# Kernel tuning notes

Measured on AMD Instinct MI355X. Metric: run time of the kernel, lower is better.

## Reference

```python
import jax, jax.numpy as jnp
import numpy as np

FEATURE_DIM = 512
PREDICATE_DIM = 2000
OBJECT_DIM = 100000
BATCH = 131072
EPS = 1e-5


def setup_inputs() -> dict:
    key = jax.random.key(0)
    ks = jax.random.split(key, 20)
    f, f2 = FEATURE_DIM, FEATURE_DIM // 2

    def w(k, shape, fan_in):
        bound = 1.0 / np.sqrt(fan_in)
        return jax.random.uniform(k, shape, jnp.float32, -bound, bound)

    inp = {
        "subj": jax.random.randint(ks[0], (BATCH,), 0, OBJECT_DIM),
        "obj": jax.random.randint(ks[1], (BATCH,), 0, OBJECT_DIM),
        "predi": jax.random.randint(ks[2], (BATCH,), 0, PREDICATE_DIM),
        # Linear weights stored as (in, out) so one_hot @ W.T == W_io[idx]
        "W1": w(ks[3], (OBJECT_DIM, f), OBJECT_DIM), "b1": w(ks[4], (f,), OBJECT_DIM),
        "g1": jnp.ones((f,), jnp.float32), "be1": jnp.zeros((f,), jnp.float32),
        "W2": w(ks[5], (OBJECT_DIM, f), OBJECT_DIM), "b2": w(ks[6], (f,), OBJECT_DIM),
        "g2": jnp.ones((f,), jnp.float32), "be2": jnp.zeros((f,), jnp.float32),
        "W3": w(ks[7], (PREDICATE_DIM, f), PREDICATE_DIM), "b3": w(ks[8], (f,), PREDICATE_DIM),
        "g3": jnp.ones((f,), jnp.float32), "be3": jnp.zeros((f,), jnp.float32),
        "W4": w(ks[9], (f2, f), f), "b4": w(ks[10], (f2,), f),
        "g4": jnp.ones((f2,), jnp.float32), "be4": jnp.zeros((f2,), jnp.float32),
        "W5": w(ks[11], (1, f2), f2), "b5": w(ks[12], (1,), f2),
    }
    return inp


def _bn(x, g, b):
    # BatchNorm1d training mode: biased variance over batch
    m = jnp.mean(x, axis=0)
    v = jnp.var(x, axis=0)
    return g * (x - m) * jax.lax.rsqrt(v + EPS) + b


def reference(subj, obj, predi,
              W1, b1, g1, be1,
              W2, b2, g2, be2,
              W3, b3, g3, be3,
              W4, b4, g4, be4,
              W5, b5):
    # one_hot(idx) @ W.T + b  ==  row gather of (in,out) weight
    s = jax.nn.relu(_bn(W1[subj] + b1, g1, be1))
    o = jax.nn.relu(_bn(W2[obj] + b2, g2, be2))
    p = jax.nn.relu(_bn(W3[predi] + b3, g3, be3))
    fused = s + p + o                                  # [B, F]
    h = jax.nn.relu(_bn(fused @ W4.T + b4, g4, be4))   # [B, F//2]
    logit = (h @ W5.T + b5).squeeze()                  # [B]
    return logit
```

## Files before the change

### kernel.cpp

```cpp
#include <hip/hip_runtime.h>

#define BATCHN 131072
#define FD 512
#define F2 256
#define NOBJ 100000
#define NPRED 2000
#define LDSTR 520

typedef __bf16 bf16x8 __attribute__((ext_vector_type(8)));
typedef float f32x4 __attribute__((ext_vector_type(4)));

__device__ __forceinline__ ushort f2bf(float f) {
  union { float f; uint u; } c; c.f = f;
  uint u = c.u;
  u += 0x7FFFu + ((u >> 16) & 1u);
  return (ushort)(u >> 16);
}

#define WS_STATS123 202752
#define WS_S4       205824
#define WS_SCSH123  238592
#define WS_SCSH4    241664
#define WS_W4BF     242176
#define WS_A1       307712
#define WS_A2       13107712
#define WS_A3       25907712
#define WS_H        26163712

__global__ __launch_bounds__(256) void k_hist(
    const int* __restrict__ subj, const int* __restrict__ obj,
    const int* __restrict__ predi, int* __restrict__ cnt)
{
  int b = blockIdx.x * 256 + threadIdx.x;
  atomicAdd(&cnt[subj[b]], 1);
  atomicAdd(&cnt[NOBJ + obj[b]], 1);
  atomicAdd(&cnt[2 * NOBJ + predi[b]], 1);
}

#define NB1 782
#define NB3 16
#define NB_SCAN (NB1 + NB1 + NB3)
__global__ __launch_bounds__(256) void k_scan123(
    const float* __restrict__ W1, const float* __restrict__ W2,
    const float* __restrict__ W3, const int* __restrict__ cnt,
    float* __restrict__ stats)
{
  int blk = blockIdx.x;
  int e, rowBase, N;
  if (blk < NB1)            { e = 0; rowBase = blk * 128;           N = NOBJ; }
  else if (blk < 2 * NB1)   { e = 1; rowBase = (blk - NB1) * 128;   N = NOBJ; }
  else                      { e = 2; rowBase = (blk - 2*NB1) * 128; N = NPRED; }
  const float* W = (e == 0) ? W1 : (e == 1 ? W2 : W3);
  const int* cn = cnt + (e == 0 ? 0 : (e == 1 ? NOBJ : 2 * NOBJ));

  __shared__ float wL[128];
  __shared__ float redS[512], redQ[512];
  int t = threadIdx.x;
  if (t < 128) { int r = rowBase + t; wL[t] = (r < N) ? (float)cn[r] : 0.f; }
  redS[t] = 0.f; redS[t + 256] = 0.f; redQ[t] = 0.f; redQ[t + 256] = 0.f;
  __syncthreads();

  int c = t & 63, rg = t >> 6;
  float s[8], q[8];
  #pragma unroll
  for (int j = 0; j < 8; ++j) { s[j] = 0.f; q[j] = 0.f; }

  #pragma unroll 8
  for (int r = rg; r < 128; r += 4) {
    int gr = rowBase + r; if (gr >= N) gr = N - 1;
    const float* row = W + (size_t)gr * FD + c * 8;
    float4 va = *(const float4*)(row);
    float4 vb = *(const float4*)(row + 4);
    float w = wL[r];
    float x[8] = {va.x, va.y, va.z, va.w, vb.x, vb.y, vb.z, vb.w};
    #pragma unroll
    for (int j = 0; j < 8; ++j) { float wx = w * x[j]; s[j] += wx; q[j] = fmaf(wx, x[j], q[j]); }
  }

  #pragma unroll
  for (int j = 0; j < 8; ++j) {
    atomicAdd(&redS[c * 8 + j], s[j]);
    atomicAdd(&redQ[c * 8 + j], q[j]);
  }
  __syncthreads();
  float* se = stats + e * 1024;
  atomicAdd(&se[t],        redS[t]);
  atomicAdd(&se[t + 256],  redS[t + 256]);
  atomicAdd(&se[512 + t],  redQ[t]);
  atomicAdd(&se[768 + t],  redQ[t + 256]);
}

__global__ void k_fin123(const float* __restrict__ stats,
                         const float* __restrict__ g1, const float* __restrict__ be1,
                         const float* __restrict__ g2, const float* __restrict__ be2,
                         const float* __restrict__ g3, const float* __restrict__ be3,
                         float* __restrict__ scsh)
{
  int e = blockIdx.x, f = threadIdx.x;
  const float* g  = (e == 0) ? g1  : (e == 1 ? g2  : g3);
  const float* be = (e == 0) ? be1 : (e == 1 ? be2 : be3);
  float S = stats[e * 1024 + f], SS = stats[e * 1024 + 512 + f];
  const float invB = 1.f / (float)BATCHN;
  float mean = S * invB;
  float var  = SS * invB - mean * mean;
  if (!(var >= 0.f && var < 1e30f)) var = 1.f;
  if (!(mean > -1e30f && mean < 1e30f)) mean = 0.f;
  float r = rsqrtf(var + 1e-5f);
  float sc = g[f] * r;
  scsh[e * 1024 + f]       = sc;
  scsh[e * 1024 + 512 + f] = be[f] - mean * sc;
}

__global__ __launch_bounds__(256) void k_convW4(const float* __restrict__ W4,
                                                ushort* __restrict__ w4bf)
{
  int i = (blockIdx.x * 256 + threadIdx.x) * 4;
  float4 v = *(const float4*)(W4 + i);
  ushort4 o = {f2bf(v.x), f2bf(v.y), f2bf(v.z), f2bf(v.w)};
  *(ushort4*)(w4bf + i) = o;
}

#define NB_A1 3125
#define NB_A3 63
#define NB_BUILD (NB_A1 + NB_A1 + NB_A3)
__global__ __launch_bounds__(256) void k_buildA(
    const float* __restrict__ W1, const float* __restrict__ W2,
    const float* __restrict__ W3, const ushort* __restrict__ w4bf,
    const int* __restrict__ cnt, const float* __restrict__ scsh,
    ushort* __restrict__ A1, ushort* __restrict__ A2, ushort* __restrict__ A3)
{
  alignas(16) __shared__ ushort tileL[32 * LDSTR];
  int blk = blockIdx.x;
  int e, rowBase, N; const float* W; ushort* A; const int* cn;
  if (blk < NB_A1)          { e = 0; rowBase = blk * 32;             N = NOBJ;  W = W1; A = A1; cn = cnt; }
  else if (blk < 2 * NB_A1) { e = 1; rowBase = (blk - NB_A1) * 32;   N = NOBJ;  W = W2; A = A2; cn = cnt + NOBJ; }
  else                      { e = 2; rowBase = (blk - 2*NB_A1) * 32; N = NPRED; W = W3; A = A3; cn = cnt + 2 * NOBJ; }

  int t = threadIdx.x;
  int c = t & 63, rg = t >> 6;
  int w = t >> 6, lane = t & 63, m = lane & 15, q = lane >> 4;

  float4 va[8], vb[8];
  #pragma unroll
  for (int u = 0; u < 8; ++u) {
    int gr = rowBase + rg + 4 * u;
    if (gr >= N) gr = N - 1;
    const float* row = W + (size_t)gr * FD + c * 8;
    va[u] = *(const float4*)(row);
    vb[u] = *(const float4*)(row + 4);
  }
  const ushort* w4p = w4bf + ((size_t)(64 * w + m)) * FD + q * 8;
  bf16x8 bc0 = *(const bf16x8*)(w4p + 0 * 16 * FD);
  bf16x8 bc1 = *(const bf16x8*)(w4p + 1 * 16 * FD);
  bf16x8 bc2 = *(const bf16x8*)(w4p + 2 * 16 * FD);
  bf16x8 bc3 = *(const bf16x8*)(w4p + 3 * 16 * FD);

  float sc[8], sh[8];
  #pragma unroll
  for (int j = 0; j < 8; ++j) {
    sc[j] = scsh[e * 1024 + c * 8 + j];
    sh[j] = scsh[e * 1024 + 512 + c * 8 + j];
  }

  #pragma unroll
  for (int u = 0; u < 8; ++u) {
    int r = rg + 4 * u;
    float x[8] = {va[u].x, va[u].y, va[u].z, va[u].w, vb[u].x, vb[u].y, vb[u].z, vb[u].w};
    union { ushort o[8]; uint4 v; } uu;
    #pragma unroll
    for (int j = 0; j < 8; ++j) {
      float v = fmaxf(fmaf(sc[j], x[j], sh[j]), 0.f);
      v = fminf(v, 60000.f);
      uu.o[j] = f2bf(v);
    }
    *(uint4*)&tileL[r * LDSTR + c * 8] = uu.v;
  }
  __syncthreads();

  f32x4 acc[2][4];
  #pragma unroll
  for (int mi = 0; mi < 2; ++mi)
    #pragma unroll
    for (int ni = 0; ni < 4; ++ni)
      acc[mi][ni] = (f32x4){0.f, 0.f, 0.f, 0.f};
  const ushort* fpL = tileL + m * LDSTR + q * 8;

  for (int kk = 0; kk < 16; ++kk) {
    int kc = kk * 32;
    bf16x8 af0 = *(const bf16x8*)(fpL + kc);
    bf16x8 af1 = *(const bf16x8*)(fpL + 16 * LDSTR + kc);
    bf16x8 bn0, bn1, bn2, bn3;
    if (kk < 15) {
      int kn = kc + 32;
      bn0 = *(const bf16x8*)(w4p + 0 * 16 * FD + kn);
      bn1 = *(const bf16x8*)(w4p + 1 * 16 * FD + kn);
      bn2 = *(const bf16x8*)(w4p + 2 * 16 * FD + kn);
      bn3 = *(const bf16x8*)(w4p + 3 * 16 * FD + kn);
    }
    acc[0][0] = __builtin_amdgcn_mfma_f32_16x16x32_bf16(af0, bc0, acc[0][0], 0, 0, 0);
    acc[1][0] = __builtin_amdgcn_mfma_f32_16x16x32_bf16(af1, bc0, acc[1][0], 0, 0, 0);
    acc[0][1] = __builtin_amdgcn_mfma_f32_16x16x32_bf16(af0, bc1, acc[0][1], 0, 0, 0);
    acc[1][1] = __builtin_amdgcn_mfma_f32_16x16x32_bf16(af1, bc1, acc[1][1], 0, 0, 0);
    acc[0][2] = __builtin_amdgcn_mfma_f32_16x16x32_bf16(af0, bc2, acc[0][2], 0, 0, 0);
    acc[1][2] = __builtin_amdgcn_mfma_f32_16x16x32_bf16(af1, bc2, acc[1][2], 0, 0, 0);
    acc[0][3] = __builtin_amdgcn_mfma_f32_16x16x32_bf16(af0, bc3, acc[0][3], 0, 0, 0);
    acc[1][3] = __builtin_amdgcn_mfma_f32_16x16x32_bf16(af1, bc3, acc[1][3], 0, 0, 0);
    bc0 = bn0; bc1 = bn1; bc2 = bn2; bc3 = bn3;
  }
  __syncthreads();

  ushort* ldsB = (ushort*)tileL;
  #pragma unroll
  for (int mi = 0; mi < 2; ++mi)
    #pragma unroll
    for (int ni = 0; ni < 4; ++ni)
      #pragma unroll
      for (int rr = 0; rr < 4; ++rr)
        ldsB[(16 * mi + 4 * q + rr) * 268 + 64 * w + 16 * ni + m] = f2bf(acc[mi][ni][rr]);
  __syncthreads();
  int hr = t >> 7, p = (t & 127) * 2;
  #pragma unroll
  for (int r = 0; r < 32; r += 2) {
    int rr = r + hr;
    int gr = rowBase + rr;
    if (gr < N && cn[gr] != 0)
      *(uint*)&A[(size_t)gr * F2 + p] = *(const uint*)&ldsB[rr * 268 + p];
  }
}

__global__ __launch_bounds__(256) void k_hstats(
    const int* __restrict__ subj, const int* __restrict__ obj,
    const int* __restrict__ predi,
    const ushort* __restrict__ A1, const ushort* __restrict__ A2,
    const ushort* __restrict__ A3, ushort* __restrict__ h,
    float* __restrict__ s4)
{
  __shared__ float colS[256], colQ[256];
  int t = threadIdx.x;
  colS[t] = 0.f; colQ[t] = 0.f;
  __syncthreads();
  int c = t & 31;
  int pair = t >> 5;
  float ls[8], lq[8];
  #pragma unroll
  for (int j = 0; j < 8; ++j) { ls[j] = 0.f; lq[j] = 0.f; }
  int base = blockIdx.x * 64;
  #pragma unroll 4
  for (int i = 0; i < 8; ++i) {
    int b = base + i * 8 + pair;
    bf16x8 v1 = *(const bf16x8*)(A1 + (size_t)subj[b]  * F2 + c * 8);
    bf16x8 v2 = *(const bf16x8*)(A2 + (size_t)obj[b]   * F2 + c * 8);
    bf16x8 v3 = *(const bf16x8*)(A3 + (size_t)predi[b] * F2 + c * 8);
    union { ushort o[8]; uint4 v; } u;
    #pragma unroll
    for (int j = 0; j < 8; ++j) {
      float hv = (float)v1[j] + (float)v2[j] + (float)v3[j];
      ls[j] += hv; lq[j] = fmaf(hv, hv, lq[j]);
      u.o[j] = f2bf(hv);
    }
    *(uint4*)&h[(size_t)b * F2 + c * 8] = u.v;
  }
  #pragma unroll
  for (int j = 0; j < 8; ++j) {
    atomicAdd(&colS[c * 8 + j], ls[j]);
    atomicAdd(&colQ[c * 8 + j], lq[j]);
  }
  __syncthreads();
  int slot = blockIdx.x & 63;
  atomicAdd(&s4[slot * 512 + t],       colS[t]);
  atomicAdd(&s4[slot * 512 + 256 + t], colQ[t]);
}

__global__ void k_fin4(const float* __restrict__ s4, const float* __restrict__ g4,
                       const float* __restrict__ be4, float* __restrict__ scsh4)
{
  int j = threadIdx.x;
  float S = 0.f, SS = 0.f;
  for (int sl = 0; sl < 64; ++sl) { S += s4[sl * 512 + j]; SS += s4[sl * 512 + 256 + j]; }
  const float invB = 1.f / (float)BATCHN;
  float mean = S * invB;
  float var  = SS * invB - mean * mean;
  if (!(var >= 0.f && var < 1e30f)) var = 1.f;
  if (!(mean > -1e30f && mean < 1e30f)) mean = 0.f;
  float r = rsqrtf(var + 1e-5f);
  float sc = g4[j] * r;
  scsh4[j]       = sc;
  scsh4[256 + j] = be4[j] - mean * sc;
}

__global__ __launch_bounds__(256) void k_final(
    const ushort* __restrict__ h, const float* __restrict__ scsh4,
    const float* __restrict__ W5, const float* __restrict__ b5,
    float* __restrict__ out)
{
  int t = threadIdx.x;
  int c = t & 31, pair = t >> 5;
  float sc4v[8], sh4v[8], w5v[8];
  #pragma unroll
  for (int j = 0; j < 8; ++j) {
    int col = c * 8 + j;
    sc4v[j] = scsh4[col];
    sh4v[j] = scsh4[256 + col];
    w5v[j]  = W5[col];
  }
  float bb = b5[0];
  int base = blockIdx.x * 64;
  #pragma unroll 4
  for (int i = 0; i < 8; ++i) {
    int b = base + i * 8 + pair;
    bf16x8 hv = *(const bf16x8*)(h + (size_t)b * F2 + c * 8);
    float acc = 0.f;
    #pragma unroll
    for (int j = 0; j < 8; ++j)
      acc += fmaxf(fmaf(sc4v[j], (float)hv[j], sh4v[j]), 0.f) * w5v[j];
    #pragma unroll
    for (int off = 1; off < 32; off <<= 1)
      acc += __shfl_xor(acc, off, 64);
    if (c == 0) out[b] = acc + bb;
  }
}

extern "C" void kernel_launch(void* const* d_in, const int* in_sizes, int n_in,
                              void* d_out, int out_size, void* d_ws, size_t ws_size,
                              hipStream_t stream)
{
  const int* subj  = (const int*)d_in[0];
  const int* obj   = (const int*)d_in[1];
  const int* predi = (const int*)d_in[2];
  const float* W1  = (const float*)d_in[3];
  const float* g1  = (const float*)d_in[5];
  const float* be1 = (const float*)d_in[6];
  const float* W2  = (const float*)d_in[7];
  const float* g2  = (const float*)d_in[9];
  const float* be2 = (const float*)d_in[10];
  const float* W3  = (const float*)d_in[11];
  const float* g3  = (const float*)d_in[13];
  const float* be3 = (const float*)d_in[14];
  const float* W4  = (const float*)d_in[15];
  const float* g4  = (const float*)d_in[17];
  const float* be4 = (const float*)d_in[18];
  const float* W5  = (const float*)d_in[19];
  const float* b5  = (const float*)d_in[20];

  float* wsf   = (float*)d_ws;
  int*   cnt   = (int*)d_ws;
  ushort* w4bf = (ushort*)(wsf + WS_W4BF);
  ushort* A1   = (ushort*)(wsf + WS_A1);
  ushort* A2   = (ushort*)(wsf + WS_A2);
  ushort* A3   = (ushort*)(wsf + WS_A3);
  ushort* hbuf = (ushort*)(wsf + WS_H);
  float* out   = (float*)d_out;

  hipMemsetAsync(d_ws, 0, WS_SCSH123 * 4, stream);
  k_hist<<<BATCHN / 256, 256, 0, stream>>>(subj, obj, predi, cnt);
  k_convW4<<<128, 256, 0, stream>>>(W4, w4bf);
  k_scan123<<<NB_SCAN, 256, 0, stream>>>(W1, W2, W3, cnt, wsf + WS_STATS123);
  k_fin123<<<3, 512, 0, stream>>>(wsf + WS_STATS123, g1, be1, g2, be2, g3, be3, wsf + WS_SCSH123);
  k_buildA<<<NB_BUILD, 256, 0, stream>>>(W1, W2, W3, w4bf, cnt, wsf + WS_SCSH123, A1, A2, A3);
  k_hstats<<<BATCHN / 64, 256, 0, stream>>>(subj, obj, predi, A1, A2, A3, hbuf, wsf + WS_S4);
  k_fin4<<<1, 256, 0, stream>>>(wsf + WS_S4, g4, be4, wsf + WS_SCSH4);
  k_final<<<BATCHN / 64, 256, 0, stream>>>(hbuf, wsf + WS_SCSH4, W5, b5, out);
}
```

Before: 826.8 us.

## Skip zero-count rows in stats scan and persist buildA with prefetch

```diff
diff --git a/kernel.cpp b/kernel.cpp
--- a/kernel.cpp
+++ b/kernel.cpp
@@ -53,29 +53,53 @@
   const float* W = (e == 0) ? W1 : (e == 1 ? W2 : W3);
   const int* cn = cnt + (e == 0 ? 0 : (e == 1 ? NOBJ : 2 * NOBJ));
 
-  __shared__ float wL[128];
+  __shared__ int cnL[128], listR[128], nkS;
   __shared__ float redS[512], redQ[512];
   int t = threadIdx.x;
-  if (t < 128) { int r = rowBase + t; wL[t] = (r < N) ? (float)cn[r] : 0.f; }
+  if (t == 0) nkS = 0;
   redS[t] = 0.f; redS[t + 256] = 0.f; redQ[t] = 0.f; redQ[t + 256] = 0.f;
   __syncthreads();
+  if (t < 128) {
+    int r = rowBase + t;
+    int cv = (r < N) ? cn[r] : 0;
+    cnL[t] = cv;
+    if (cv > 0) { int p = atomicAdd(&nkS, 1); listR[p] = t; }
+  }
+  __syncthreads();
+  int nk = nkS;
 
   int c = t & 63, rg = t >> 6;
   float s[8], q[8];
   #pragma unroll
   for (int j = 0; j < 8; ++j) { s[j] = 0.f; q[j] = 0.f; }
 
-  #pragma unroll 8
-  for (int r = rg; r < 128; r += 4) {
-    int gr = rowBase + r; if (gr >= N) gr = N - 1;
-    const float* row = W + (size_t)gr * FD + c * 8;
-    float4 va = *(const float4*)(row);
-    float4 vb = *(const float4*)(row + 4);
-    float w = wL[r];
-    float x[8] = {va.x, va.y, va.z, va.w, vb.x, vb.y, vb.z, vb.w};
-    #pragma unroll
-    for (int j = 0; j < 8; ++j) { float wx = w * x[j]; s[j] += wx; q[j] = fmaf(wx, x[j], q[j]); }
-  }
+  #define SCAN_ACC(w_, va_, vb_) { \
+    float x_[8] = {va_.x, va_.y, va_.z, va_.w, vb_.x, vb_.y, vb_.z, vb_.w}; \
+    _Pragma("unroll") \
+    for (int j = 0; j < 8; ++j) { float wx = w_ * x_[j]; s[j] += wx; q[j] = fmaf(wx, x_[j], q[j]); } }
+
+  int ii = rg;
+  for (; ii + 12 < nk; ii += 16) {
+    int r0 = listR[ii], r1 = listR[ii + 4], r2 = listR[ii + 8], r3 = listR[ii + 12];
+    const float* p0 = W + (size_t)(rowBase + r0) * FD + c * 8;
+    const float* p1 = W + (size_t)(rowBase + r1) * FD + c * 8;
+    const float* p2 = W + (size_t)(rowBase + r2) * FD + c * 8;
+    const float* p3 = W + (size_t)(rowBase + r3) * FD + c * 8;
+    float4 a0 = *(const float4*)(p0), b0 = *(const float4*)(p0 + 4);
+    float4 a1 = *(const float4*)(p1), b1 = *(const float4*)(p1 + 4);
+    float4 a2 = *(const float4*)(p2), b2 = *(const float4*)(p2 + 4);
+    float4 a3 = *(const float4*)(p3), b3 = *(const float4*)(p3 + 4);
+    float w0 = (float)cnL[r0], w1 = (float)cnL[r1], w2 = (float)cnL[r2], w3 = (float)cnL[r3];
+    SCAN_ACC(w0, a0, b0); SCAN_ACC(w1, a1, b1); SCAN_ACC(w2, a2, b2); SCAN_ACC(w3, a3, b3);
+  }
+  for (; ii < nk; ii += 4) {
+    int r0 = listR[ii];
+    const float* p0 = W + (size_t)(rowBase + r0) * FD + c * 8;
+    float4 a0 = *(const float4*)(p0), b0 = *(const float4*)(p0 + 4);
+    float w0 = (float)cnL[r0];
+    SCAN_ACC(w0, a0, b0);
+  }
+  #undef SCAN_ACC
 
   #pragma unroll
   for (int j = 0; j < 8; ++j) {
@@ -123,108 +147,145 @@
 #define NB_A1 3125
 #define NB_A3 63
 #define NB_BUILD (NB_A1 + NB_A1 + NB_A3)
+#define G_BUILD 512
+
 __global__ __launch_bounds__(256) void k_buildA(
     const float* __restrict__ W1, const float* __restrict__ W2,
     const float* __restrict__ W3, const ushort* __restrict__ w4bf,
     const int* __restrict__ cnt, const float* __restrict__ scsh,
     ushort* __restrict__ A1, ushort* __restrict__ A2, ushort* __restrict__ A3)
 {
-  alignas(16) __shared__ ushort tileL[32 * LDSTR];
-  int blk = blockIdx.x;
-  int e, rowBase, N; const float* W; ushort* A; const int* cn;
-  if (blk < NB_A1)          { e = 0; rowBase = blk * 32;             N = NOBJ;  W = W1; A = A1; cn = cnt; }
-  else if (blk < 2 * NB_A1) { e = 1; rowBase = (blk - NB_A1) * 32;   N = NOBJ;  W = W2; A = A2; cn = cnt + NOBJ; }
-  else                      { e = 2; rowBase = (blk - 2*NB_A1) * 32; N = NPRED; W = W3; A = A3; cn = cnt + 2 * NOBJ; }
-
+  alignas(16) __shared__ ushort buf[2][32 * LDSTR];
+  __shared__ int cnOk[2][32];
   int t = threadIdx.x;
   int c = t & 63, rg = t >> 6;
   int w = t >> 6, lane = t & 63, m = lane & 15, q = lane >> 4;
-
+  const ushort* w4p = w4bf + ((size_t)(64 * w + m)) * FD + q * 8;
+
+  auto tileInfo = [&](int blk, int& e, int& rowBase, int& N,
+                      const float*& W, ushort*& A, const int*& cn) {
+    if (blk < NB_A1)          { e = 0; rowBase = blk * 32;             N = NOBJ;  W = W1; A = A1; cn = cnt; }
+    else if (blk < 2 * NB_A1) { e = 1; rowBase = (blk - NB_A1) * 32;   N = NOBJ;  W = W2; A = A2; cn = cnt + NOBJ; }
+    else                      { e = 2; rowBase = (blk - 2*NB_A1) * 32; N = NPRED; W = W3; A = A3; cn = cnt + 2 * NOBJ; }
+  };
+
+  int tt = (int)blockIdx.x;
   float4 va[8], vb[8];
-  #pragma unroll
-  for (int u = 0; u < 8; ++u) {
-    int gr = rowBase + rg + 4 * u;
-    if (gr >= N) gr = N - 1;
-    const float* row = W + (size_t)gr * FD + c * 8;
-    va[u] = *(const float4*)(row);
-    vb[u] = *(const float4*)(row + 4);
-  }
-  const ushort* w4p = w4bf + ((size_t)(64 * w + m)) * FD + q * 8;
-  bf16x8 bc0 = *(const bf16x8*)(w4p + 0 * 16 * FD);
-  bf16x8 bc1 = *(const bf16x8*)(w4p + 1 * 16 * FD);
-  bf16x8 bc2 = *(const bf16x8*)(w4p + 2 * 16 * FD);
-  bf16x8 bc3 = *(const bf16x8*)(w4p + 3 * 16 * FD);
-
-  float sc[8], sh[8];
-  #pragma unroll
-  for (int j = 0; j < 8; ++j) {
-    sc[j] = scsh[e * 1024 + c * 8 + j];
-    sh[j] = scsh[e * 1024 + 512 + c * 8 + j];
-  }
-
-  #pragma unroll
-  for (int u = 0; u < 8; ++u) {
-    int r = rg + 4 * u;
-    float x[8] = {va[u].x, va[u].y, va[u].z, va[u].w, vb[u].x, vb[u].y, vb[u].z, vb[u].w};
-    union { ushort o[8]; uint4 v; } uu;
+  {
+    int e, rowBase, N; const float* W; ushort* A; const int* cn;
+    tileInfo(tt, e, rowBase, N, W, A, cn);
+    #pragma unroll
+    for (int u = 0; u < 8; ++u) {
+      int gr = rowBase + rg + 4 * u; if (gr >= N) gr = N - 1;
+      const float* row = W + (size_t)gr * FD + c * 8;
+      va[u] = *(const float4*)(row);
+      vb[u] = *(const float4*)(row + 4);
+    }
+  }
+
+  int cur = 0;
+  for (; tt < NB_BUILD; tt += G_BUILD, cur ^= 1) {
+    int e, rowBase, N; const float* W; ushort* A; const int* cn;
+    tileInfo(tt, e, rowBase, N, W, A, cn);
+
+    if (t < 32) {
+      int gr = rowBase + t;
+      cnOk[cur][t] = (gr < N) && (cn[gr] != 0);
+    }
+    float sc[8], sh[8];
     #pragma unroll
     for (int j = 0; j < 8; ++j) {
-      float v = fmaxf(fmaf(sc[j], x[j], sh[j]), 0.f);
-      v = fminf(v, 60000.f);
-      uu.o[j] = f2bf(v);
-    }
-    *(uint4*)&tileL[r * LDSTR + c * 8] = uu.v;
-  }
-  __syncthreads();
-
-  f32x4 acc[2][4];
-  #pragma unroll
-  for (int mi = 0; mi < 2; ++mi)
-    #pragma unroll
-    for (int ni = 0; ni < 4; ++ni)
-      acc[mi][ni] = (f32x4){0.f, 0.f, 0.f, 0.f};
-  const ushort* fpL = tileL + m * LDSTR + q * 8;
-
-  for (int kk = 0; kk < 16; ++kk) {
-    int kc = kk * 32;
-    bf16x8 af0 = *(const bf16x8*)(fpL + kc);
-    bf16x8 af1 = *(const bf16x8*)(fpL + 16 * LDSTR + kc);
-    bf16x8 bn0, bn1, bn2, bn3;
-    if (kk < 15) {
-      int kn = kc + 32;
-      bn0 = *(const bf16x8*)(w4p + 0 * 16 * FD + kn);
-      bn1 = *(const bf16x8*)(w4p + 1 * 16 * FD + kn);
-      bn2 = *(const bf16x8*)(w4p + 2 * 16 * FD + kn);
-      bn3 = *(const bf16x8*)(w4p + 3 * 16 * FD + kn);
-    }
-    acc[0][0] = __builtin_amdgcn_mfma_f32_16x16x32_bf16(af0, bc0, acc[0][0], 0, 0, 0);
-    acc[1][0] = __builtin_amdgcn_mfma_f32_16x16x32_bf16(af1, bc0, acc[1][0], 0, 0, 0);
-    acc[0][1] = __builtin_amdgcn_mfma_f32_16x16x32_bf16(af0, bc1, acc[0][1], 0, 0, 0);
-    acc[1][1] = __builtin_amdgcn_mfma_f32_16x16x32_bf16(af1, bc1, acc[1][1], 0, 0, 0);
-    acc[0][2] = __builtin_amdgcn_mfma_f32_16x16x32_bf16(af0, bc2, acc[0][2], 0, 0, 0);
-    acc[1][2] = __builtin_amdgcn_mfma_f32_16x16x32_bf16(af1, bc2, acc[1][2], 0, 0, 0);
-    acc[0][3] = __builtin_amdgcn_mfma_f32_16x16x32_bf16(af0, bc3, acc[0][3], 0, 0, 0);
-    acc[1][3] = __builtin_amdgcn_mfma_f32_16x16x32_bf16(af1, bc3, acc[1][3], 0, 0, 0);
-    bc0 = bn0; bc1 = bn1; bc2 = bn2; bc3 = bn3;
-  }
-  __syncthreads();
-
-  ushort* ldsB = (ushort*)tileL;
-  #pragma unroll
-  for (int mi = 0; mi < 2; ++mi)
-    #pragma unroll
-    for (int ni = 0; ni < 4; ++ni)
+      sc[j] = scsh[e * 1024 + c * 8 + j];
+      sh[j] = scsh[e * 1024 + 512 + c * 8 + j];
+    }
+
+    #pragma unroll
+    for (int u = 0; u < 8; ++u) {
+      int r = rg + 4 * u;
+      float x[8] = {va[u].x, va[u].y, va[u].z, va[u].w, vb[u].x, vb[u].y, vb[u].z, vb[u].w};
+      union { ushort o[8]; uint4 v; } uu;
       #pragma unroll
-      for (int rr = 0; rr < 4; ++rr)
-        ldsB[(16 * mi + 4 * q + rr) * 268 + 64 * w + 16 * ni + m] = f2bf(acc[mi][ni][rr]);
-  __syncthreads();
-  int hr = t >> 7, p = (t & 127) * 2;
-  #pragma unroll
-  for (int r = 0; r < 32; r += 2) {
-    int rr = r + hr;
-    int gr = rowBase + rr;
-    if (gr < N && cn[gr] != 0)
-      *(uint*)&A[(size_t)gr * F2 + p] = *(const uint*)&ldsB[rr * 268 + p];
+      for (int j = 0; j < 8; ++j) {
+        float v = fmaxf(fmaf(sc[j], x[j], sh[j]), 0.f);
+        v = fminf(v, 60000.f);
+        uu.o[j] = f2bf(v);
+      }
+      *(uint4*)&buf[cur][r * LDSTR + c * 8] = uu.v;
+    }
+
+    bf16x8 bc0 = *(const bf16x8*)(w4p + 0 * 16 * FD);
+    bf16x8 bc1 = *(const bf16x8*)(w4p + 1 * 16 * FD);
+    bf16x8 bc2 = *(const bf16x8*)(w4p + 2 * 16 * FD);
+    bf16x8 bc3 = *(const bf16x8*)(w4p + 3 * 16 * FD);
+
+    asm volatile("s_waitcnt lgkmcnt(0)" ::: "memory");
+    __builtin_amdgcn_s_barrier();
+
+    f32x4 acc[2][4];
+    #pragma unroll
+    for (int mi = 0; mi < 2; ++mi)
+      #pragma unroll
+      for (int ni = 0; ni < 4; ++ni)
+        acc[mi][ni] = (f32x4){0.f, 0.f, 0.f, 0.f};
+    const ushort* fpL = &buf[cur][m * LDSTR + q * 8];
+
+    for (int kk = 0; kk < 16; ++kk) {
+      int kc = kk * 32;
+      bf16x8 af0 = *(const bf16x8*)(fpL + kc);
+      bf16x8 af1 = *(const bf16x8*)(fpL + 16 * LDSTR + kc);
+      bf16x8 bn0, bn1, bn2, bn3;
+      if (kk < 15) {
+        int kn = kc + 32;
+        bn0 = *(const bf16x8*)(w4p + 0 * 16 * FD + kn);
+        bn1 = *(const bf16x8*)(w4p + 1 * 16 * FD + kn);
+        bn2 = *(const bf16x8*)(w4p + 2 * 16 * FD + kn);
+        bn3 = *(const bf16x8*)(w4p + 3 * 16 * FD + kn);
+      }
+      acc[0][0] = __builtin_amdgcn_mfma_f32_16x16x32_bf16(af0, bc0, acc[0][0], 0, 0, 0);
+      acc[1][0] = __builtin_amdgcn_mfma_f32_16x16x32_bf16(af1, bc0, acc[1][0], 0, 0, 0);
+      acc[0][1] = __builtin_amdgcn_mfma_f32_16x16x32_bf16(af0, bc1, acc[0][1], 0, 0, 0);
+      acc[1][1] = __builtin_amdgcn_mfma_f32_16x16x32_bf16(af1, bc1, acc[1][1], 0, 0, 0);
+      acc[0][2] = __builtin_amdgcn_mfma_f32_16x16x32_bf16(af0, bc2, acc[0][2], 0, 0, 0);
+      acc[1][2] = __builtin_amdgcn_mfma_f32_16x16x32_bf16(af1, bc2, acc[1][2], 0, 0, 0);
+      acc[0][3] = __builtin_amdgcn_mfma_f32_16x16x32_bf16(af0, bc3, acc[0][3], 0, 0, 0);
+      acc[1][3] = __builtin_amdgcn_mfma_f32_16x16x32_bf16(af1, bc3, acc[1][3], 0, 0, 0);
+      bc0 = bn0; bc1 = bn1; bc2 = bn2; bc3 = bn3;
+    }
+
+    if (tt + G_BUILD < NB_BUILD) {
+      int e2, rowBase2, N2; const float* Wn; ushort* An; const int* cnn;
+      tileInfo(tt + G_BUILD, e2, rowBase2, N2, Wn, An, cnn);
+      #pragma unroll
+      for (int u = 0; u < 8; ++u) {
+        int gr = rowBase2 + rg + 4 * u; if (gr >= N2) gr = N2 - 1;
+        const float* row = Wn + (size_t)gr * FD + c * 8;
+        va[u] = *(const float4*)(row);
+        vb[u] = *(const float4*)(row + 4);
+      }
+    }
+
+    asm volatile("s_waitcnt lgkmcnt(0)" ::: "memory");
+    __builtin_amdgcn_s_barrier();
+
+    ushort* ldsB = buf[cur];
+    #pragma unroll
+    for (int mi = 0; mi < 2; ++mi)
+      #pragma unroll
+      for (int ni = 0; ni < 4; ++ni)
+        #pragma unroll
+        for (int rr = 0; rr < 4; ++rr)
+          ldsB[(16 * mi + 4 * q + rr) * 268 + 64 * w + 16 * ni + m] = f2bf(acc[mi][ni][rr]);
+
+    asm volatile("s_waitcnt lgkmcnt(0)" ::: "memory");
+    __builtin_amdgcn_s_barrier();
+
+    int hr = t >> 7, p = (t & 127) * 2;
+    #pragma unroll
+    for (int r = 0; r < 32; r += 2) {
+      int rr = r + hr;
+      if (cnOk[cur][rr])
+        *(uint*)&A[(size_t)(rowBase + rr) * F2 + p] = *(const uint*)&ldsB[rr * 268 + p];
+    }
   }
 }
 
@@ -356,7 +417,7 @@
   k_convW4<<<128, 256, 0, stream>>>(W4, w4bf);
   k_scan123<<<NB_SCAN, 256, 0, stream>>>(W1, W2, W3, cnt, wsf + WS_STATS123);
   k_fin123<<<3, 512, 0, stream>>>(wsf + WS_STATS123, g1, be1, g2, be2, g3, be3, wsf + WS_SCSH123);
-  k_buildA<<<NB_BUILD, 256, 0, stream>>>(W1, W2, W3, w4bf, cnt, wsf + WS_SCSH123, A1, A2, A3);
+  k_buildA<<<G_BUILD, 256, 0, stream>>>(W1, W2, W3, w4bf, cnt, wsf + WS_SCSH123, A1, A2, A3);
   k_hstats<<<BATCHN / 64, 256, 0, stream>>>(subj, obj, predi, A1, A2, A3, hbuf, wsf + WS_S4);
   k_fin4<<<1, 256, 0, stream>>>(wsf + WS_S4, g4, be4, wsf + WS_SCSH4);
   k_final<<<BATCHN / 64, 256, 0, stream>>>(hbuf, wsf + WS_SCSH4, W5, b5, out);
```

Result: slower. 869.0 us (+5.1%).

## Convert embedding tables to bf16 during stats scan and reuse in GEMM

Applied to the files above, without the earlier changes.

```diff
diff --git a/kernel.cpp b/kernel.cpp
--- a/kernel.cpp
+++ b/kernel.cpp
@@ -6,6 +6,7 @@
 #define NOBJ 100000
 #define NPRED 2000
 #define LDSTR 520
+#define RPB 128
 
 typedef __bf16 bf16x8 __attribute__((ext_vector_type(8)));
 typedef float f32x4 __attribute__((ext_vector_type(4)));
@@ -22,10 +23,11 @@
 #define WS_SCSH123  238592
 #define WS_SCSH4    241664
 #define WS_W4BF     242176
-#define WS_A1       307712
-#define WS_A2       13107712
-#define WS_A3       25907712
-#define WS_H        26163712
+#define WS_WBF      307712
+#define WS_A1       25907712
+#define WS_A2       38707712
+#define WS_A3       51507712
+#define WS_H        WS_WBF
 
 __global__ __launch_bounds__(256) void k_hist(
     const int* __restrict__ subj, const int* __restrict__ obj,
@@ -37,44 +39,36 @@
   atomicAdd(&cnt[2 * NOBJ + predi[b]], 1);
 }
 
-#define NB1 782
-#define NB3 16
-#define NB_SCAN (NB1 + NB1 + NB3)
-__global__ __launch_bounds__(256) void k_scan123(
-    const float* __restrict__ W1, const float* __restrict__ W2,
-    const float* __restrict__ W3, const int* __restrict__ cnt,
-    float* __restrict__ stats)
-{
-  int blk = blockIdx.x;
-  int e, rowBase, N;
-  if (blk < NB1)            { e = 0; rowBase = blk * 128;           N = NOBJ; }
-  else if (blk < 2 * NB1)   { e = 1; rowBase = (blk - NB1) * 128;   N = NOBJ; }
-  else                      { e = 2; rowBase = (blk - 2*NB1) * 128; N = NPRED; }
-  const float* W = (e == 0) ? W1 : (e == 1 ? W2 : W3);
-  const int* cn = cnt + (e == 0 ? 0 : (e == 1 ? NOBJ : 2 * NOBJ));
-
-  __shared__ float wL[128];
+__global__ __launch_bounds__(256) void k_scanconv(
+    const float* __restrict__ W, const int* __restrict__ cn,
+    float* __restrict__ statsE, ushort* __restrict__ wbf, int N)
+{
   __shared__ float redS[512], redQ[512];
   int t = threadIdx.x;
-  if (t < 128) { int r = rowBase + t; wL[t] = (r < N) ? (float)cn[r] : 0.f; }
   redS[t] = 0.f; redS[t + 256] = 0.f; redQ[t] = 0.f; redQ[t + 256] = 0.f;
   __syncthreads();
-
   int c = t & 63, rg = t >> 6;
+  int base = blockIdx.x * RPB;
+  int end = min(N, base + RPB);
   float s[8], q[8];
   #pragma unroll
   for (int j = 0; j < 8; ++j) { s[j] = 0.f; q[j] = 0.f; }
 
-  #pragma unroll 8
-  for (int r = rg; r < 128; r += 4) {
-    int gr = rowBase + r; if (gr >= N) gr = N - 1;
-    const float* row = W + (size_t)gr * FD + c * 8;
+  #pragma unroll 4
+  for (int r = base + rg; r < end; r += 4) {
+    const float* row = W + (size_t)r * FD + c * 8;
     float4 va = *(const float4*)(row);
     float4 vb = *(const float4*)(row + 4);
-    float w = wL[r];
+    float wv = (float)cn[r];
     float x[8] = {va.x, va.y, va.z, va.w, vb.x, vb.y, vb.z, vb.w};
-    #pragma unroll
-    for (int j = 0; j < 8; ++j) { float wx = w * x[j]; s[j] += wx; q[j] = fmaf(wx, x[j], q[j]); }
+    union { ushort o[8]; uint4 v; } u;
+    #pragma unroll
+    for (int j = 0; j < 8; ++j) {
+      float wx = wv * x[j];
+      s[j] += wx; q[j] = fmaf(wx, x[j], q[j]);
+      u.o[j] = f2bf(x[j]);
+    }
+    if (wv > 0.f) *(uint4*)&wbf[(size_t)r * FD + c * 8] = u.v;
   }
 
   #pragma unroll
@@ -83,23 +77,18 @@
     atomicAdd(&redQ[c * 8 + j], q[j]);
   }
   __syncthreads();
-  float* se = stats + e * 1024;
-  atomicAdd(&se[t],        redS[t]);
-  atomicAdd(&se[t + 256],  redS[t + 256]);
-  atomicAdd(&se[512 + t],  redQ[t]);
-  atomicAdd(&se[768 + t],  redQ[t + 256]);
-}
-
-__global__ void k_fin123(const float* __restrict__ stats,
-                         const float* __restrict__ g1, const float* __restrict__ be1,
-                         const float* __restrict__ g2, const float* __restrict__ be2,
-                         const float* __restrict__ g3, const float* __restrict__ be3,
-                         float* __restrict__ scsh)
-{
-  int e = blockIdx.x, f = threadIdx.x;
-  const float* g  = (e == 0) ? g1  : (e == 1 ? g2  : g3);
-  const float* be = (e == 0) ? be1 : (e == 1 ? be2 : be3);
-  float S = stats[e * 1024 + f], SS = stats[e * 1024 + 512 + f];
+  atomicAdd(&statsE[t],        redS[t]);
+  atomicAdd(&statsE[t + 256],  redS[t + 256]);
+  atomicAdd(&statsE[512 + t],  redQ[t]);
+  atomicAdd(&statsE[768 + t],  redQ[t + 256]);
+}
+
+__global__ void k_fin1(const float* __restrict__ statsE,
+                       const float* __restrict__ g, const float* __restrict__ be,
+                       float* __restrict__ scshE)
+{
+  int f = threadIdx.x;
+  float S = statsE[f], SS = statsE[512 + f];
   const float invB = 1.f / (float)BATCHN;
   float mean = S * invB;
   float var  = SS * invB - mean * mean;
@@ -107,8 +96,8 @@
   if (!(mean > -1e30f && mean < 1e30f)) mean = 0.f;
   float r = rsqrtf(var + 1e-5f);
   float sc = g[f] * r;
-  scsh[e * 1024 + f]       = sc;
-  scsh[e * 1024 + 512 + f] = be[f] - mean * sc;
+  scshE[f]       = sc;
+  scshE[512 + f] = be[f] - mean * sc;
 }
 
 __global__ __launch_bounds__(256) void k_convW4(const float* __restrict__ W4,
@@ -120,34 +109,25 @@
   *(ushort4*)(w4bf + i) = o;
 }
 
-#define NB_A1 3125
-#define NB_A3 63
-#define NB_BUILD (NB_A1 + NB_A1 + NB_A3)
-__global__ __launch_bounds__(256) void k_buildA(
-    const float* __restrict__ W1, const float* __restrict__ W2,
-    const float* __restrict__ W3, const ushort* __restrict__ w4bf,
-    const int* __restrict__ cnt, const float* __restrict__ scsh,
-    ushort* __restrict__ A1, ushort* __restrict__ A2, ushort* __restrict__ A3)
+__global__ __launch_bounds__(256) void k_gemmA(
+    const ushort* __restrict__ wbf, const ushort* __restrict__ w4bf,
+    const int* __restrict__ cn, const float* __restrict__ scshE,
+    ushort* __restrict__ A, int N)
 {
   alignas(16) __shared__ ushort tileL[32 * LDSTR];
-  int blk = blockIdx.x;
-  int e, rowBase, N; const float* W; ushort* A; const int* cn;
-  if (blk < NB_A1)          { e = 0; rowBase = blk * 32;             N = NOBJ;  W = W1; A = A1; cn = cnt; }
-  else if (blk < 2 * NB_A1) { e = 1; rowBase = (blk - NB_A1) * 32;   N = NOBJ;  W = W2; A = A2; cn = cnt + NOBJ; }
-  else                      { e = 2; rowBase = (blk - 2*NB_A1) * 32; N = NPRED; W = W3; A = A3; cn = cnt + 2 * NOBJ; }
-
+  __shared__ int cnOk[32];
   int t = threadIdx.x;
+  int rowBase = blockIdx.x * 32;
   int c = t & 63, rg = t >> 6;
   int w = t >> 6, lane = t & 63, m = lane & 15, q = lane >> 4;
 
-  float4 va[8], vb[8];
+  if (t < 32) { int gr = rowBase + t; cnOk[t] = (gr < N) && (cn[gr] != 0); }
+
+  uint4 st[8];
   #pragma unroll
   for (int u = 0; u < 8; ++u) {
-    int gr = rowBase + rg + 4 * u;
-    if (gr >= N) gr = N - 1;
-    const float* row = W + (size_t)gr * FD + c * 8;
-    va[u] = *(const float4*)(row);
-    vb[u] = *(const float4*)(row + 4);
+    int gr = rowBase + rg + 4 * u; if (gr >= N) gr = N - 1;
+    st[u] = *(const uint4*)&wbf[(size_t)gr * FD + c * 8];
   }
   const ushort* w4p = w4bf + ((size_t)(64 * w + m)) * FD + q * 8;
   bf16x8 bc0 = *(const bf16x8*)(w4p + 0 * 16 * FD);
@@ -158,22 +138,23 @@
   float sc[8], sh[8];
   #pragma unroll
   for (int j = 0; j < 8; ++j) {
-    sc[j] = scsh[e * 1024 + c * 8 + j];
-    sh[j] = scsh[e * 1024 + 512 + c * 8 + j];
+    sc[j] = scshE[c * 8 + j];
+    sh[j] = scshE[512 + c * 8 + j];
   }
 
   #pragma unroll
   for (int u = 0; u < 8; ++u) {
     int r = rg + 4 * u;
-    float x[8] = {va[u].x, va[u].y, va[u].z, va[u].w, vb[u].x, vb[u].y, vb[u].z, vb[u].w};
-    union { ushort o[8]; uint4 v; } uu;
+    union { uint4 v; ushort o[8]; } in; in.v = st[u];
+    union { ushort o[8]; uint4 v; } out;
     #pragma unroll
     for (int j = 0; j < 8; ++j) {
-      float v = fmaxf(fmaf(sc[j], x[j], sh[j]), 0.f);
+      union { uint uu; float f; } cv; cv.uu = (uint)in.o[j] << 16;
+      float v = fmaxf(fmaf(sc[j], cv.f, sh[j]), 0.f);
       v = fminf(v, 60000.f);
-      uu.o[j] = f2bf(v);
+      out.o[j] = f2bf(v);
     }
-    *(uint4*)&tileL[r * LDSTR + c * 8] = uu.v;
+    *(uint4*)&tileL[r * LDSTR + c * 8] = out.v;
   }
   __syncthreads();
 
@@ -222,9 +203,8 @@
   #pragma unroll
   for (int r = 0; r < 32; r += 2) {
     int rr = r + hr;
-    int gr = rowBase + rr;
-    if (gr < N && cn[gr] != 0)
-      *(uint*)&A[(size_t)gr * F2 + p] = *(const uint*)&ldsB[rr * 268 + p];
+    if (cnOk[rr])
+      *(uint*)&A[(size_t)(rowBase + rr) * F2 + p] = *(const uint*)&ldsB[rr * 268 + p];
   }
 }
 
@@ -345,6 +325,7 @@
   float* wsf   = (float*)d_ws;
   int*   cnt   = (int*)d_ws;
   ushort* w4bf = (ushort*)(wsf + WS_W4BF);
+  ushort* wbf  = (ushort*)(wsf + WS_WBF);
   ushort* A1   = (ushort*)(wsf + WS_A1);
   ushort* A2   = (ushort*)(wsf + WS_A2);
   ushort* A3   = (ushort*)(wsf + WS_A3);
@@ -354,9 +335,19 @@
   hipMemsetAsync(d_ws, 0, WS_SCSH123 * 4, stream);
   k_hist<<<BATCHN / 256, 256, 0, stream>>>(subj, obj, predi, cnt);
   k_convW4<<<128, 256, 0, stream>>>(W4, w4bf);
-  k_scan123<<<NB_SCAN, 256, 0, stream>>>(W1, W2, W3, cnt, wsf + WS_STATS123);
-  k_fin123<<<3, 512, 0, stream>>>(wsf + WS_STATS123, g1, be1, g2, be2, g3, be3, wsf + WS_SCSH123);
-  k_buildA<<<NB_BUILD, 256, 0, stream>>>(W1, W2, W3, w4bf, cnt, wsf + WS_SCSH123, A1, A2, A3);
+
+  k_scanconv<<<(NOBJ + RPB - 1) / RPB, 256, 0, stream>>>(W1, cnt, wsf + WS_STATS123, wbf, NOBJ);
+  k_fin1<<<1, 512, 0, stream>>>(wsf + WS_STATS123, g1, be1, wsf + WS_SCSH123);
+  k_gemmA<<<NOBJ / 32, 256, 0, stream>>>(wbf, w4bf, cnt, wsf + WS_SCSH123, A1, NOBJ);
+
+  k_scanconv<<<(NOBJ + RPB - 1) / RPB, 256, 0, stream>>>(W2, cnt + NOBJ, wsf + WS_STATS123 + 1024, wbf, NOBJ);
+  k_fin1<<<1, 512, 0, stream>>>(wsf + WS_STATS123 + 1024, g2, be2, wsf + WS_SCSH123 + 1024);
+  k_gemmA<<<NOBJ / 32, 256, 0, stream>>>(wbf, w4bf, cnt + NOBJ, wsf + WS_SCSH123 + 1024, A2, NOBJ);
+
+  k_scanconv<<<(NPRED + RPB - 1) / RPB, 256, 0, stream>>>(W3, cnt + 2 * NOBJ, wsf + WS_STATS123 + 2048, wbf, NPRED);
+  k_fin1<<<1, 512, 0, stream>>>(wsf + WS_STATS123 + 2048, g3, be3, wsf + WS_SCSH123 + 2048);
+  k_gemmA<<<(NPRED + 31) / 32, 256, 0, stream>>>(wbf, w4bf, cnt + 2 * NOBJ, wsf + WS_SCSH123 + 2048, A3, NPRED);
+
   k_hstats<<<BATCHN / 64, 256, 0, stream>>>(subj, obj, predi, A1, A2, A3, hbuf, wsf + WS_S4);
   k_fin4<<<1, 256, 0, stream>>>(wsf + WS_S4, g4, be4, wsf + WS_SCSH4);
   k_final<<<BATCHN / 64, 256, 0, stream>>>(hbuf, wsf + WS_SCSH4, W5, b5, out);
```

New measurement: 890.3 us. 1.08x slower.
